# Performance work log

Hardware: AMD Instinct MI355X
Metric: run time of the kernel (lower is better)

Reference implementation:

```python
import jax, jax.numpy as jnp
import numpy as np

N = 50000
NUM_NEIGHBORS = 16
E = N * NUM_NEIGHBORS
NDIM_IN, EDIM, NDIM_OUT = 128, 64, 128


def setup_inputs() -> dict:
    key = jax.random.key(0)
    k1, k2, k3, k4, k5, k6, k7 = jax.random.split(key, 7)
    nfeats = jax.random.normal(k1, (N, 1, NDIM_IN), dtype=jnp.float32)
    efeats = jax.random.normal(k2, (E, 1, EDIM), dtype=jnp.float32)
    W_msg = jax.random.normal(k3, (NDIM_OUT, NDIM_IN + EDIM), dtype=jnp.float32) * 0.05
    b_msg = jax.random.normal(k4, (NDIM_OUT,), dtype=jnp.float32) * 0.05
    W_apply = jax.random.normal(k5, (NDIM_OUT, NDIM_IN + NDIM_OUT), dtype=jnp.float32) * 0.05
    b_apply = jax.random.normal(k6, (NDIM_OUT,), dtype=jnp.float32) * 0.05
    src_idx = jax.random.randint(k7, (E,), 0, N, dtype=jnp.int32)
    # sampled graph: each node is the destination of exactly NUM_NEIGHBORS edges
    dst_idx = jnp.repeat(jnp.arange(N, dtype=jnp.int32), NUM_NEIGHBORS)
    return {"nfeats": nfeats, "efeats": efeats, "W_msg": W_msg, "b_msg": b_msg,
            "W_apply": W_apply, "b_apply": b_apply, "src_idx": src_idx, "dst_idx": dst_idx}


def reference(nfeats, efeats, W_msg, b_msg, W_apply, b_apply, src_idx, dst_idx):
    n = nfeats.shape[0]
    # message: W_msg(cat([src_h, edge_h], -1))  -> [E, 1, ndim_out]
    src_h = nfeats[src_idx]                                   # [E,1,Din] gather
    msg_in = jnp.concatenate([src_h, efeats], axis=-1)        # [E,1,Din+Edim]
    m = jnp.einsum('eid,od->eio', msg_in, W_msg) + b_msg      # [E,1,Dout]
    # mean aggregation over incoming edges per destination node
    msum = jax.ops.segment_sum(m[:, 0, :], dst_idx, num_segments=n)   # [N,Dout]
    cnt = jax.ops.segment_sum(jnp.ones((m.shape[0],), m.dtype), dst_idx, num_segments=n)
    h_neigh = (msum / jnp.maximum(cnt, 1.0)[:, None])[:, None, :]     # [N,1,Dout]
    # apply: relu(W_apply(cat([nfeats, h_neigh], -1)))
    app_in = jnp.concatenate([nfeats, h_neigh], axis=-1)      # [N,1,Din+Dout]
    h_new = jax.nn.relu(jnp.einsum('nid,od->nio', app_in, W_apply) + b_apply)
    return h_new
```

## Files before the change

### kernel.cpp

```cpp
#include <hip/hip_runtime.h>

#define N_NODES 50000
#define NN 16
#define K_FUSED 320

typedef __attribute__((ext_vector_type(8))) short bfrag8;
typedef __attribute__((ext_vector_type(4))) float facc4;

__device__ __forceinline__ unsigned short f2bf(float f) {
    unsigned int u = __builtin_bit_cast(unsigned int, f);
    u = (u + 0x7fffu + ((u >> 16) & 1u)) >> 16;
    return (unsigned short)u;
}
__device__ __forceinline__ float bflo(unsigned v) {
    return __builtin_bit_cast(float, v << 16);
}
__device__ __forceinline__ float bfhi(unsigned v) {
    return __builtin_bit_cast(float, v & 0xffff0000u);
}

__global__ void wfuse_kernel(const float* __restrict__ W_msg,
                             const float* __restrict__ b_msg,
                             const float* __restrict__ W_apply,
                             const float* __restrict__ b_apply,
                             unsigned short* __restrict__ Wf,
                             float* __restrict__ bias_f) {
    __shared__ float sWa[128];
    const int o = blockIdx.x;
    const int tid = threadIdx.x;
    if (tid < 128) sWa[tid] = W_apply[o * 256 + 128 + tid];
    __syncthreads();
    if (tid < 128) Wf[o * K_FUSED + tid] = f2bf(W_apply[o * 256 + tid]);
    if (tid < 192) {
        float acc = 0.f;
        #pragma unroll 8
        for (int p = 0; p < 128; ++p) acc += sWa[p] * W_msg[p * 192 + tid];
        Wf[o * K_FUSED + 128 + tid] = f2bf(acc);
    } else if (tid == 192) {
        float acc = b_apply[o];
        for (int p = 0; p < 128; ++p) acc += sWa[p] * b_msg[p];
        bias_f[o] = acc;
    }
}

__global__ __launch_bounds__(256)
void nconv_kernel(const float* __restrict__ nf, uint4* __restrict__ nfb) {
    const long i = (long)blockIdx.x * 256 + threadIdx.x;
    const float4* p = (const float4*)nf + 2 * i;
    const float4 a = p[0], b = p[1];
    uint4 o;
    o.x = (unsigned)f2bf(a.x) | ((unsigned)f2bf(a.y) << 16);
    o.y = (unsigned)f2bf(a.z) | ((unsigned)f2bf(a.w) << 16);
    o.z = (unsigned)f2bf(b.x) | ((unsigned)f2bf(b.y) << 16);
    o.w = (unsigned)f2bf(b.z) | ((unsigned)f2bf(b.w) << 16);
    nfb[i] = o;
}

__global__ __launch_bounds__(256)
void fused_kernel(const float* __restrict__ efeats,
                  const int* __restrict__ src_idx,
                  const unsigned short* __restrict__ nfb,
                  const uint4* __restrict__ WfQ,
                  const float* __restrict__ bias_f,
                  float* __restrict__ out) {
    __shared__ unsigned short Xs[64 * 200];
    const int tid = threadIdx.x;
    const int wave = tid >> 6, lane = tid & 63;
    const int nodeBase = blockIdx.x * 64;

    for (int nl = 0; nl < 16; ++nl) {
        const int n = nodeBase + wave * 16 + nl;
        unsigned short* row = Xs + (wave * 16 + nl) * 200;
        if (n < N_NODES) {
            const long e0 = (long)n * NN;
            float s0 = 0.f, s1 = 0.f, tacc = 0.f;
            #pragma unroll
            for (int j = 0; j < NN; ++j) {
                const int src = src_idx[e0 + j];
                const unsigned v = *(const unsigned*)(nfb + (long)src * 128 + 2 * lane);
                s0 += bflo(v); s1 += bfhi(v);
                tacc += efeats[(e0 + j) * 64 + lane];
            }
            const float inv = 1.f / 16.f;
            ((unsigned*)row)[lane] =
                (unsigned)f2bf(s0 * inv) | ((unsigned)f2bf(s1 * inv) << 16);
            row[128 + lane] = f2bf(tacc * inv);
        } else {
            ((unsigned*)row)[lane] = 0u;
            row[128 + lane] = 0;
        }
    }
    __syncthreads();

    const int quad = lane >> 4, mcol = lane & 15;
    const int nrow = nodeBase + wave * 16 + mcol;
    const int nclamp = nrow < N_NODES ? nrow : N_NODES - 1;
    const char* xg = (const char*)(nfb + (long)nclamp * 128);
    const char* xl = (const char*)(Xs + (wave * 16 + mcol) * 200);
    const char* wb = (const char*)WfQ;

    facc4 acc[8] = {};
    #pragma unroll
    for (int ks = 0; ks < 10; ++ks) {
        bfrag8 a;
        if (ks < 4)
            a = __builtin_bit_cast(bfrag8, *(const uint4*)(xg + ks * 64 + quad * 16));
        else
            a = __builtin_bit_cast(bfrag8, *(const uint4*)(xl + (ks - 4) * 64 + quad * 16));
        #pragma unroll
        for (int t = 0; t < 8; ++t) {
            const uint4 bv = *(const uint4*)(wb + (t * 16 + mcol) * 640 + ks * 64 + quad * 16);
            const bfrag8 b = __builtin_bit_cast(bfrag8, bv);
            acc[t] = __builtin_amdgcn_mfma_f32_16x16x32_bf16(a, b, acc[t], 0, 0, 0);
        }
    }

    #pragma unroll
    for (int t = 0; t < 8; ++t) {
        const int ocol = t * 16 + mcol;
        const float bb = bias_f[ocol];
        #pragma unroll
        for (int r = 0; r < 4; ++r) {
            const int node = nodeBase + wave * 16 + quad * 4 + r;
            if (node < N_NODES) {
                const float v = acc[t][r] + bb;
                out[(long)node * 128 + ocol] = v > 0.f ? v : 0.f;
            }
        }
    }
}

extern "C" void kernel_launch(void* const* d_in, const int* in_sizes, int n_in,
                              void* d_out, int out_size, void* d_ws, size_t ws_size,
                              hipStream_t stream) {
    const float* nfeats  = (const float*)d_in[0];
    const float* efeats  = (const float*)d_in[1];
    const float* W_msg   = (const float*)d_in[2];
    const float* b_msg   = (const float*)d_in[3];
    const float* W_apply = (const float*)d_in[4];
    const float* b_apply = (const float*)d_in[5];
    const int*   src_idx = (const int*)d_in[6];
    float* out = (float*)d_out;

    char* ws = (char*)d_ws;
    unsigned short* Wf     = (unsigned short*)ws;
    float*          bias_f = (float*)(ws + 81920);
    unsigned short* nfb    = (unsigned short*)(ws + 82432);

    wfuse_kernel<<<128, 256, 0, stream>>>(W_msg, b_msg, W_apply, b_apply, Wf, bias_f);
    nconv_kernel<<<3125, 256, 0, stream>>>(nfeats, (uint4*)nfb);
    fused_kernel<<<(N_NODES + 63) / 64, 256, 0, stream>>>(
        efeats, src_idx, nfb, (const uint4*)Wf, bias_f, out);
}
```

Measured before the change: 375.3 us.

## Merge setup kernels and halve node tile with split-wave gather

Combines the weight-fusion and node bf16 conversion kernels into one launch, which removes a kernel launch boundary. In the main kernel each block now handles 32 nodes instead of 64. The gather splits each wave into two halves that process alternate edges with 8-byte loads, broadcasts src indices via shuffle, and reduces the halves with xor-shuffles. The MFMA stage splits output columns across wave pairs, and the change adds an occupancy hint. Together these aim to raise memory-level parallelism and occupancy in the gather-bound phase, at the cost of extra shuffles and of loading each weight tile for twice as many blocks.

```diff
diff --git a/kernel.cpp b/kernel.cpp
--- a/kernel.cpp
+++ b/kernel.cpp
@@ -19,87 +19,108 @@
     return __builtin_bit_cast(float, v & 0xffff0000u);
 }
 
-__global__ void wfuse_kernel(const float* __restrict__ W_msg,
-                             const float* __restrict__ b_msg,
-                             const float* __restrict__ W_apply,
-                             const float* __restrict__ b_apply,
-                             unsigned short* __restrict__ Wf,
-                             float* __restrict__ bias_f) {
+__global__ __launch_bounds__(256)
+void setup_kernel(const float* __restrict__ W_msg,
+                  const float* __restrict__ b_msg,
+                  const float* __restrict__ W_apply,
+                  const float* __restrict__ b_apply,
+                  const float* __restrict__ nf,
+                  unsigned short* __restrict__ Wf,
+                  float* __restrict__ bias_f,
+                  uint4* __restrict__ nfb) {
     __shared__ float sWa[128];
-    const int o = blockIdx.x;
     const int tid = threadIdx.x;
-    if (tid < 128) sWa[tid] = W_apply[o * 256 + 128 + tid];
-    __syncthreads();
-    if (tid < 128) Wf[o * K_FUSED + tid] = f2bf(W_apply[o * 256 + tid]);
-    if (tid < 192) {
-        float acc = 0.f;
-        #pragma unroll 8
-        for (int p = 0; p < 128; ++p) acc += sWa[p] * W_msg[p * 192 + tid];
-        Wf[o * K_FUSED + 128 + tid] = f2bf(acc);
-    } else if (tid == 192) {
-        float acc = b_apply[o];
-        for (int p = 0; p < 128; ++p) acc += sWa[p] * b_msg[p];
-        bias_f[o] = acc;
+    if (blockIdx.x < 128) {
+        const int o = blockIdx.x;
+        if (tid < 128) sWa[tid] = W_apply[o * 256 + 128 + tid];
+        __syncthreads();
+        if (tid < 128) Wf[o * K_FUSED + tid] = f2bf(W_apply[o * 256 + tid]);
+        if (tid < 192) {
+            float acc = 0.f;
+            #pragma unroll 8
+            for (int p = 0; p < 128; ++p) acc += sWa[p] * W_msg[p * 192 + tid];
+            Wf[o * K_FUSED + 128 + tid] = f2bf(acc);
+        } else if (tid == 192) {
+            float acc = b_apply[o];
+            for (int p = 0; p < 128; ++p) acc += sWa[p] * b_msg[p];
+            bias_f[o] = acc;
+        }
+    } else {
+        const long i = (long)(blockIdx.x - 128) * 256 + tid;
+        const float4* p = (const float4*)nf + 2 * i;
+        const float4 a = p[0], b = p[1];
+        uint4 o;
+        o.x = (unsigned)f2bf(a.x) | ((unsigned)f2bf(a.y) << 16);
+        o.y = (unsigned)f2bf(a.z) | ((unsigned)f2bf(a.w) << 16);
+        o.z = (unsigned)f2bf(b.x) | ((unsigned)f2bf(b.y) << 16);
+        o.w = (unsigned)f2bf(b.z) | ((unsigned)f2bf(b.w) << 16);
+        nfb[i] = o;
     }
 }
 
-__global__ __launch_bounds__(256)
-void nconv_kernel(const float* __restrict__ nf, uint4* __restrict__ nfb) {
-    const long i = (long)blockIdx.x * 256 + threadIdx.x;
-    const float4* p = (const float4*)nf + 2 * i;
-    const float4 a = p[0], b = p[1];
-    uint4 o;
-    o.x = (unsigned)f2bf(a.x) | ((unsigned)f2bf(a.y) << 16);
-    o.y = (unsigned)f2bf(a.z) | ((unsigned)f2bf(a.w) << 16);
-    o.z = (unsigned)f2bf(b.x) | ((unsigned)f2bf(b.y) << 16);
-    o.w = (unsigned)f2bf(b.z) | ((unsigned)f2bf(b.w) << 16);
-    nfb[i] = o;
-}
-
-__global__ __launch_bounds__(256)
+__global__ __launch_bounds__(256, 6)
 void fused_kernel(const float* __restrict__ efeats,
                   const int* __restrict__ src_idx,
                   const unsigned short* __restrict__ nfb,
                   const uint4* __restrict__ WfQ,
                   const float* __restrict__ bias_f,
                   float* __restrict__ out) {
-    __shared__ unsigned short Xs[64 * 200];
+    __shared__ unsigned short Xs[32 * 200];
     const int tid = threadIdx.x;
     const int wave = tid >> 6, lane = tid & 63;
-    const int nodeBase = blockIdx.x * 64;
+    const int nodeBase = blockIdx.x * 32;
 
-    for (int nl = 0; nl < 16; ++nl) {
-        const int n = nodeBase + wave * 16 + nl;
-        unsigned short* row = Xs + (wave * 16 + nl) * 200;
+    const int g = lane >> 5;
+    const int m = lane & 31;
+
+    #pragma unroll
+    for (int nl = 0; nl < 8; ++nl) {
+        const int rrow = wave * 8 + nl;
+        const int n = nodeBase + rrow;
+        unsigned short* row = Xs + rrow * 200;
+        float s0 = 0.f, s1 = 0.f, s2 = 0.f, s3 = 0.f, t0 = 0.f, t1 = 0.f;
         if (n < N_NODES) {
             const long e0 = (long)n * NN;
-            float s0 = 0.f, s1 = 0.f, tacc = 0.f;
+            const int sj = src_idx[e0 + (lane & 15)];
             #pragma unroll
-            for (int j = 0; j < NN; ++j) {
-                const int src = src_idx[e0 + j];
-                const unsigned v = *(const unsigned*)(nfb + (long)src * 128 + 2 * lane);
-                s0 += bflo(v); s1 += bfhi(v);
-                tacc += efeats[(e0 + j) * 64 + lane];
+            for (int i = 0; i < 8; ++i) {
+                const int j = 2 * i + g;
+                const int srcj = __shfl(sj, j, 64);
+                const uint2 sv = *(const uint2*)(nfb + (long)srcj * 128 + 4 * m);
+                const float2 tv = *(const float2*)(efeats + (e0 + j) * 64 + 2 * m);
+                s0 += bflo(sv.x); s1 += bfhi(sv.x);
+                s2 += bflo(sv.y); s3 += bfhi(sv.y);
+                t0 += tv.x; t1 += tv.y;
             }
+        }
+        s0 += __shfl_xor(s0, 32, 64);
+        s1 += __shfl_xor(s1, 32, 64);
+        s2 += __shfl_xor(s2, 32, 64);
+        s3 += __shfl_xor(s3, 32, 64);
+        t0 += __shfl_xor(t0, 32, 64);
+        t1 += __shfl_xor(t1, 32, 64);
+        if (g == 0) {
             const float inv = 1.f / 16.f;
-            ((unsigned*)row)[lane] =
-                (unsigned)f2bf(s0 * inv) | ((unsigned)f2bf(s1 * inv) << 16);
-            row[128 + lane] = f2bf(tacc * inv);
-        } else {
-            ((unsigned*)row)[lane] = 0u;
-            row[128 + lane] = 0;
+            uint2 sp;
+            sp.x = (unsigned)f2bf(s0 * inv) | ((unsigned)f2bf(s1 * inv) << 16);
+            sp.y = (unsigned)f2bf(s2 * inv) | ((unsigned)f2bf(s3 * inv) << 16);
+            ((uint2*)row)[m] = sp;
+            ((unsigned*)(row + 128))[m] =
+                (unsigned)f2bf(t0 * inv) | ((unsigned)f2bf(t1 * inv) << 16);
         }
     }
     __syncthreads();
 
     const int quad = lane >> 4, mcol = lane & 15;
-    const int nrow = nodeBase + wave * 16 + mcol;
+    const int mt = wave & 1;
+    const int cg = wave >> 1;
+    const int nrow = nodeBase + mt * 16 + mcol;
     const int nclamp = nrow < N_NODES ? nrow : N_NODES - 1;
     const char* xg = (const char*)(nfb + (long)nclamp * 128);
-    const char* xl = (const char*)(Xs + (wave * 16 + mcol) * 200);
+    const char* xl = (const char*)(Xs + (mt * 16 + mcol) * 200);
     const char* wb = (const char*)WfQ;
 
-    facc4 acc[8] = {};
+    facc4 acc[4] = {};
     #pragma unroll
     for (int ks = 0; ks < 10; ++ks) {
         bfrag8 a;
@@ -108,20 +129,21 @@
         else
             a = __builtin_bit_cast(bfrag8, *(const uint4*)(xl + (ks - 4) * 64 + quad * 16));
         #pragma unroll
-        for (int t = 0; t < 8; ++t) {
-            const uint4 bv = *(const uint4*)(wb + (t * 16 + mcol) * 640 + ks * 64 + quad * 16);
+        for (int t = 0; t < 4; ++t) {
+            const int orow = cg * 64 + t * 16 + mcol;
+            const uint4 bv = *(const uint4*)(wb + orow * 640 + ks * 64 + quad * 16);
             const bfrag8 b = __builtin_bit_cast(bfrag8, bv);
             acc[t] = __builtin_amdgcn_mfma_f32_16x16x32_bf16(a, b, acc[t], 0, 0, 0);
         }
     }
 
     #pragma unroll
-    for (int t = 0; t < 8; ++t) {
-        const int ocol = t * 16 + mcol;
+    for (int t = 0; t < 4; ++t) {
+        const int ocol = cg * 64 + t * 16 + mcol;
         const float bb = bias_f[ocol];
         #pragma unroll
         for (int r = 0; r < 4; ++r) {
-            const int node = nodeBase + wave * 16 + quad * 4 + r;
+            const int node = nodeBase + mt * 16 + quad * 4 + r;
             if (node < N_NODES) {
                 const float v = acc[t][r] + bb;
                 out[(long)node * 128 + ocol] = v > 0.f ? v : 0.f;
@@ -147,8 +169,8 @@
     float*          bias_f = (float*)(ws + 81920);
     unsigned short* nfb    = (unsigned short*)(ws + 82432);
 
-    wfuse_kernel<<<128, 256, 0, stream>>>(W_msg, b_msg, W_apply, b_apply, Wf, bias_f);
-    nconv_kernel<<<3125, 256, 0, stream>>>(nfeats, (uint4*)nfb);
-    fused_kernel<<<(N_NODES + 63) / 64, 256, 0, stream>>>(
+    setup_kernel<<<128 + 3125, 256, 0, stream>>>(
+        W_msg, b_msg, W_apply, b_apply, nfeats, Wf, bias_f, (uint4*)nfb);
+    fused_kernel<<<(N_NODES + 31) / 32, 256, 0, stream>>>(
         efeats, src_idx, nfb, (const uint4*)Wf, bias_f, out);
 }
```

Result: faster. 358.1 us (-4.6%).

## Split gather/aggregation into its own kernel and merge weight-fuse with bf16 convert

Applied to the files above, without the earlier changes.

Gather-and-mean aggregation moves out of the fused kernel into a separate prep kernel with one node per wave, over many more blocks. It writes a bf16 staging buffer in global memory that a new MFMA apply kernel reads in place of LDS. The weight-fusion and nfeats bf16 conversion kernels become one launch. This aims to raise parallelism and latency hiding for the gather-bound phase, at the cost of an extra global round trip for the staged rows and an extra launch.

```diff
diff --git a/kernel.cpp b/kernel.cpp
--- a/kernel.cpp
+++ b/kernel.cpp
@@ -1,8 +1,10 @@
 #include <hip/hip_runtime.h>
 
 #define N_NODES 50000
+#define NP 50048
 #define NN 16
 #define K_FUSED 320
+#define ST_SHORTS 192
 
 typedef __attribute__((ext_vector_type(8))) short bfrag8;
 typedef __attribute__((ext_vector_type(4))) float facc4;
@@ -19,84 +21,92 @@
     return __builtin_bit_cast(float, v & 0xffff0000u);
 }
 
-__global__ void wfuse_kernel(const float* __restrict__ W_msg,
-                             const float* __restrict__ b_msg,
-                             const float* __restrict__ W_apply,
-                             const float* __restrict__ b_apply,
-                             unsigned short* __restrict__ Wf,
-                             float* __restrict__ bias_f) {
+__global__ __launch_bounds__(256)
+void setup_kernel(const float* __restrict__ W_msg,
+                  const float* __restrict__ b_msg,
+                  const float* __restrict__ W_apply,
+                  const float* __restrict__ b_apply,
+                  const float* __restrict__ nf,
+                  unsigned short* __restrict__ Wf,
+                  float* __restrict__ bias_f,
+                  uint4* __restrict__ nfb) {
     __shared__ float sWa[128];
-    const int o = blockIdx.x;
     const int tid = threadIdx.x;
-    if (tid < 128) sWa[tid] = W_apply[o * 256 + 128 + tid];
-    __syncthreads();
-    if (tid < 128) Wf[o * K_FUSED + tid] = f2bf(W_apply[o * 256 + tid]);
-    if (tid < 192) {
-        float acc = 0.f;
-        #pragma unroll 8
-        for (int p = 0; p < 128; ++p) acc += sWa[p] * W_msg[p * 192 + tid];
-        Wf[o * K_FUSED + 128 + tid] = f2bf(acc);
-    } else if (tid == 192) {
-        float acc = b_apply[o];
-        for (int p = 0; p < 128; ++p) acc += sWa[p] * b_msg[p];
-        bias_f[o] = acc;
+    if (blockIdx.x < 128) {
+        const int o = blockIdx.x;
+        if (tid < 128) sWa[tid] = W_apply[o * 256 + 128 + tid];
+        __syncthreads();
+        if (tid < 128) Wf[o * K_FUSED + tid] = f2bf(W_apply[o * 256 + tid]);
+        if (tid < 192) {
+            float acc = 0.f;
+            #pragma unroll 8
+            for (int p = 0; p < 128; ++p) acc += sWa[p] * W_msg[p * 192 + tid];
+            Wf[o * K_FUSED + 128 + tid] = f2bf(acc);
+        } else if (tid == 192) {
+            float acc = b_apply[o];
+            for (int p = 0; p < 128; ++p) acc += sWa[p] * b_msg[p];
+            bias_f[o] = acc;
+        }
+    } else {
+        const long i = (long)(blockIdx.x - 128) * 256 + tid;
+        const float4* p = (const float4*)nf + 2 * i;
+        const float4 a = p[0], b = p[1];
+        uint4 o;
+        o.x = (unsigned)f2bf(a.x) | ((unsigned)f2bf(a.y) << 16);
+        o.y = (unsigned)f2bf(a.z) | ((unsigned)f2bf(a.w) << 16);
+        o.z = (unsigned)f2bf(b.x) | ((unsigned)f2bf(b.y) << 16);
+        o.w = (unsigned)f2bf(b.z) | ((unsigned)f2bf(b.w) << 16);
+        nfb[i] = o;
     }
 }
 
 __global__ __launch_bounds__(256)
-void nconv_kernel(const float* __restrict__ nf, uint4* __restrict__ nfb) {
-    const long i = (long)blockIdx.x * 256 + threadIdx.x;
-    const float4* p = (const float4*)nf + 2 * i;
-    const float4 a = p[0], b = p[1];
-    uint4 o;
-    o.x = (unsigned)f2bf(a.x) | ((unsigned)f2bf(a.y) << 16);
-    o.y = (unsigned)f2bf(a.z) | ((unsigned)f2bf(a.w) << 16);
-    o.z = (unsigned)f2bf(b.x) | ((unsigned)f2bf(b.y) << 16);
-    o.w = (unsigned)f2bf(b.z) | ((unsigned)f2bf(b.w) << 16);
-    nfb[i] = o;
+void prep_kernel(const float* __restrict__ efeats,
+                 const int* __restrict__ src_idx,
+                 const unsigned short* __restrict__ nfb,
+                 unsigned short* __restrict__ X_st) {
+    const int wave = threadIdx.x >> 6;
+    const int lane = threadIdx.x & 63;
+    const int n = blockIdx.x * 4 + wave;
+    if (n >= NP) return;
+    unsigned short* row = X_st + (long)n * ST_SHORTS;
+
+    if (n < N_NODES) {
+        const long e0 = (long)n * NN;
+        float s0 = 0.f, s1 = 0.f;
+        float tacc = 0.f;
+        #pragma unroll
+        for (int j = 0; j < NN; ++j) {
+            const int src = src_idx[e0 + j];
+            const unsigned v = *(const unsigned*)(nfb + (long)src * 128 + 2 * lane);
+            s0 += bflo(v); s1 += bfhi(v);
+            tacc += efeats[(e0 + j) * 64 + lane];
+        }
+        const float inv = 1.f / 16.f;
+        ((unsigned*)row)[lane] =
+            (unsigned)f2bf(s0 * inv) | ((unsigned)f2bf(s1 * inv) << 16);
+        row[128 + lane] = f2bf(tacc * inv);
+    } else {
+        ((unsigned*)row)[lane] = 0u;
+        row[128 + lane] = 0;
+    }
 }
 
 __global__ __launch_bounds__(256)
-void fused_kernel(const float* __restrict__ efeats,
-                  const int* __restrict__ src_idx,
+void apply_kernel(const unsigned short* __restrict__ X_st,
                   const unsigned short* __restrict__ nfb,
                   const uint4* __restrict__ WfQ,
                   const float* __restrict__ bias_f,
                   float* __restrict__ out) {
-    __shared__ unsigned short Xs[64 * 200];
     const int tid = threadIdx.x;
     const int wave = tid >> 6, lane = tid & 63;
-    const int nodeBase = blockIdx.x * 64;
+    const int quad = lane >> 4, mcol = lane & 15;
+    const int node0 = blockIdx.x * 64 + wave * 16;
 
-    for (int nl = 0; nl < 16; ++nl) {
-        const int n = nodeBase + wave * 16 + nl;
-        unsigned short* row = Xs + (wave * 16 + nl) * 200;
-        if (n < N_NODES) {
-            const long e0 = (long)n * NN;
-            float s0 = 0.f, s1 = 0.f, tacc = 0.f;
-            #pragma unroll
-            for (int j = 0; j < NN; ++j) {
-                const int src = src_idx[e0 + j];
-                const unsigned v = *(const unsigned*)(nfb + (long)src * 128 + 2 * lane);
-                s0 += bflo(v); s1 += bfhi(v);
-                tacc += efeats[(e0 + j) * 64 + lane];
-            }
-            const float inv = 1.f / 16.f;
-            ((unsigned*)row)[lane] =
-                (unsigned)f2bf(s0 * inv) | ((unsigned)f2bf(s1 * inv) << 16);
-            row[128 + lane] = f2bf(tacc * inv);
-        } else {
-            ((unsigned*)row)[lane] = 0u;
-            row[128 + lane] = 0;
-        }
-    }
-    __syncthreads();
-
-    const int quad = lane >> 4, mcol = lane & 15;
-    const int nrow = nodeBase + wave * 16 + mcol;
+    const int nrow = node0 + mcol;
     const int nclamp = nrow < N_NODES ? nrow : N_NODES - 1;
     const char* xg = (const char*)(nfb + (long)nclamp * 128);
-    const char* xl = (const char*)(Xs + (wave * 16 + mcol) * 200);
+    const char* xs = (const char*)(X_st + (long)nrow * ST_SHORTS);
     const char* wb = (const char*)WfQ;
 
     facc4 acc[8] = {};
@@ -106,7 +116,7 @@
         if (ks < 4)
             a = __builtin_bit_cast(bfrag8, *(const uint4*)(xg + ks * 64 + quad * 16));
         else
-            a = __builtin_bit_cast(bfrag8, *(const uint4*)(xl + (ks - 4) * 64 + quad * 16));
+            a = __builtin_bit_cast(bfrag8, *(const uint4*)(xs + (ks - 4) * 64 + quad * 16));
         #pragma unroll
         for (int t = 0; t < 8; ++t) {
             const uint4 bv = *(const uint4*)(wb + (t * 16 + mcol) * 640 + ks * 64 + quad * 16);
@@ -121,7 +131,7 @@
         const float bb = bias_f[ocol];
         #pragma unroll
         for (int r = 0; r < 4; ++r) {
-            const int node = nodeBase + wave * 16 + quad * 4 + r;
+            const int node = node0 + quad * 4 + r;
             if (node < N_NODES) {
                 const float v = acc[t][r] + bb;
                 out[(long)node * 128 + ocol] = v > 0.f ? v : 0.f;
@@ -146,9 +156,11 @@
     unsigned short* Wf     = (unsigned short*)ws;
     float*          bias_f = (float*)(ws + 81920);
     unsigned short* nfb    = (unsigned short*)(ws + 82432);
+    unsigned short* X_st   = (unsigned short*)(ws + 82432 + (long)NP * 256);
 
-    wfuse_kernel<<<128, 256, 0, stream>>>(W_msg, b_msg, W_apply, b_apply, Wf, bias_f);
-    nconv_kernel<<<3125, 256, 0, stream>>>(nfeats, (uint4*)nfb);
-    fused_kernel<<<(N_NODES + 63) / 64, 256, 0, stream>>>(
-        efeats, src_idx, nfb, (const uint4*)Wf, bias_f, out);
+    setup_kernel<<<128 + 3125, 256, 0, stream>>>(
+        W_msg, b_msg, W_apply, b_apply, nfeats, Wf, bias_f, (uint4*)nfb);
+    prep_kernel<<<NP / 4, 256, 0, stream>>>(efeats, src_idx, nfb, X_st);
+    apply_kernel<<<NP / 64, 256, 0, stream>>>(
+        X_st, nfb, (const uint4*)Wf, bias_f, out);
 }
```

After: 370.0 us. Within noise of the previous version (-1.4%).
